# Kernel tuning notes

Measured on AMD Instinct MI355X. Metric: run time of the kernel, lower is better.

## Reference

```python
import jax, jax.numpy as jnp
import numpy as np

N_NODES = 50000
N_EDGES = 800000
IN_DIM = 256
HID_DIM = 128
N_LAYERS = 3


def setup_inputs() -> dict:
    key = jax.random.key(0)
    ks = jax.random.split(key, 7)
    s = 0.05
    x = jax.random.normal(ks[0], (N_NODES, IN_DIM), dtype=jnp.float32)
    edge_index = jax.random.randint(ks[1], (2, N_EDGES), 0, N_NODES, dtype=jnp.int64)
    W_enc = jax.random.normal(ks[2], (HID_DIM, IN_DIM), dtype=jnp.float32) * s
    b_enc = jax.random.normal(ks[3], (HID_DIM,), dtype=jnp.float32) * s
    W_l = jax.random.normal(ks[4], (N_LAYERS, HID_DIM, HID_DIM), dtype=jnp.float32) * s
    b_l = jax.random.normal(ks[5], (N_LAYERS, HID_DIM), dtype=jnp.float32) * s
    W_r = jax.random.normal(ks[6], (N_LAYERS, HID_DIM, HID_DIM), dtype=jnp.float32) * s
    return {"x": x, "edge_index": edge_index, "W_enc": W_enc, "b_enc": b_enc,
            "W_l": W_l, "b_l": b_l, "W_r": W_r}


def reference(x, edge_index, W_enc, b_enc, W_l, b_l, W_r):
    # eval mode: dropout is identity
    n = x.shape[0]
    src, dst = edge_index[0], edge_index[1]
    # encode: Linear(in_dim -> hid_dim)
    h = x @ W_enc.T + b_enc  # [N, H]
    # in-degree for mean aggregation (nodes with no in-edges -> 0 output)
    deg = jax.ops.segment_sum(jnp.ones((src.shape[0],), h.dtype), dst, num_segments=n)
    denom = jnp.maximum(deg, 1.0)[:, None]  # [N, 1]
    for i in range(W_l.shape[0]):
        # mean of source-node features over incoming edges
        agg = jax.ops.segment_sum(h[src], dst, num_segments=n) / denom  # [N, H]
        # SAGEConv: lin_l(agg) + lin_r(h)  (lin_r has no bias)
        h = agg @ W_l[i].T + b_l[i] + h @ W_r[i].T
    return h
```

## Files before the change

kernel.cpp:

```cpp
#include <hip/hip_runtime.h>

#define N_NODES 50000
#define N_EDGES 800000
#define IN_DIM 256
#define HID_DIM 128
#define ROWTILES 3125
#define ENC_BLOCKS 1024
#define WCVT_BLOCKS 48
#define CNT_BLOCKS 256
#define EDGES_PER_CB 3125
#define LYR_GRID 256
#define CAP_E 352
#define TPAD 3136

typedef float f4 __attribute__((ext_vector_type(4)));
typedef float f32x4 __attribute__((ext_vector_type(4)));
typedef float vf2 __attribute__((ext_vector_type(2)));
typedef short bf16x8 __attribute__((ext_vector_type(8)));

__device__ __forceinline__ unsigned short f2bf(float f) {
    unsigned u = __builtin_bit_cast(unsigned, f);
    return (unsigned short)((u + 0x7fffu + ((u >> 16) & 1u)) >> 16);
}
__device__ __forceinline__ unsigned pk2(float a, float b) {
    return (unsigned)f2bf(a) | ((unsigned)f2bf(b) << 16);
}
__device__ __forceinline__ bf16x8 cvt8(f4 a, f4 b) {
    union { bf16x8 v; unsigned u[4]; } r;
    r.u[0] = pk2(a[0], a[1]);
    r.u[1] = pk2(a[2], a[3]);
    r.u[2] = pk2(b[0], b[1]);
    r.u[3] = pk2(b[2], b[3]);
    return r.v;
}
__device__ __forceinline__ vf2 dec8(unsigned short t) {
    return __builtin_amdgcn_cvt_pk_f32_fp8((int)(unsigned)t, false);
}
__device__ __forceinline__ void gl_lds16(const void* g, void* l) {
    __builtin_amdgcn_global_load_lds(
        (const __attribute__((address_space(1))) unsigned int*)g,
        (__attribute__((address_space(3))) unsigned int*)l, 16, 0, 0);
}


__global__ __launch_bounds__(256) void k_pre(const int* __restrict__ dst,
                                             int* __restrict__ Cm,
                                             const float* __restrict__ Wl, const float* __restrict__ Wr,
                                             unsigned short* __restrict__ wlrbf,
                                             const float* __restrict__ x,
                                             const float* __restrict__ Wenc,
                                             const float* __restrict__ bias,
                                             unsigned short* __restrict__ hout,
                                             unsigned char* __restrict__ f8out) {
    __shared__ int smem_i[8192];
    int tid = threadIdx.x;
    if (blockIdx.x < WCVT_BLOCKS) {
        int idx = blockIdx.x * 2048 + tid * 8;
        const float* srcp = (idx < 49152) ? (Wl + idx) : (Wr + (idx - 49152));
        const f4* g = (const f4*)srcp;
        *(bf16x8*)(wlrbf + idx) = cvt8(g[0], g[1]);
        return;
    }
    if (blockIdx.x >= WCVT_BLOCKS + ENC_BLOCKS) {
        int c = blockIdx.x - WCVT_BLOCKS - ENC_BLOCKS;
        int* cnt = smem_i;
        for (int i = tid; i < TPAD; i += 256) cnt[i] = 0;
        __syncthreads();
        const int* dp = dst + c * EDGES_PER_CB;
        for (int i = tid; i < EDGES_PER_CB; i += 256)
            atomicAdd(&cnt[dp[i] >> 4], 1);
        __syncthreads();
        int* crow = Cm + (size_t)c * TPAD;
        for (int t = tid; t < TPAD; t += 256) crow[t] = cnt[t];
        return;
    }
    float* xsf = (float*)smem_i;
    int bid = blockIdx.x - WCVT_BLOCKS;
    int lane = tid & 63;
    int wv = tid >> 6;
    int colbase = wv * 32;
    int lr = lane & 15;
    int kh = (lane >> 4) * 8;
    int khB = kh * 4;
    int swz = (lr & 7) << 4;

    bf16x8 bfr[2][8];
#pragma unroll
    for (int n = 0; n < 2; ++n) {
        const float* wp = Wenc + (size_t)(colbase + n * 16 + lr) * IN_DIM + kh;
#pragma unroll
        for (int s = 0; s < 8; ++s) {
            const f4* g = (const f4*)(wp + s * 32);
            bfr[n][s] = cvt8(g[0], g[1]);
        }
    }
    float bias0 = bias[colbase + lr];
    float bias1 = bias[colbase + 16 + lr];

    int pb = 0;
    for (int rt = bid; rt < ROWTILES; rt += ENC_BLOCKS, pb ^= 1) {
#pragma unroll
        for (int jj = 0; jj < 4; ++jj) {
            int j = wv * 4 + jj;
            const char* gsrc = (const char*)(x + (size_t)(rt * 16 + j) * IN_DIM)
                               + ((lane * 16) ^ ((j & 7) << 4));
            gl_lds16(gsrc, (char*)(xsf + pb * 4096) + j * 1024);
        }
        __syncthreads();

        const char* xb = (const char*)(xsf + pb * 4096) + lr * 1024;
        bf16x8 afr[8];
#pragma unroll
        for (int s = 0; s < 8; ++s) {
            int lo = khB + s * 128;
            f4 a = *(const f4*)(xb + ((lo) ^ swz));
            f4 b = *(const f4*)(xb + ((lo + 16) ^ swz));
            afr[s] = cvt8(a, b);
        }
        f32x4 acc0 = {0.f, 0.f, 0.f, 0.f}, acc1 = {0.f, 0.f, 0.f, 0.f};
#pragma unroll
        for (int s = 0; s < 8; ++s) {
            acc0 = __builtin_amdgcn_mfma_f32_16x16x32_bf16(afr[s], bfr[0][s], acc0, 0, 0, 0);
            acc1 = __builtin_amdgcn_mfma_f32_16x16x32_bf16(afr[s], bfr[1][s], acc1, 0, 0, 0);
        }
        int rbase = rt * 16 + (lane >> 4) * 4;
#pragma unroll
        for (int r = 0; r < 4; ++r) {
            float v0 = acc0[r] + bias0, v1 = acc1[r] + bias1;
            unsigned short* op = hout + (size_t)(rbase + r) * HID_DIM;
            op[colbase + lr] = f2bf(v0);
            op[colbase + 16 + lr] = f2bf(v1);
            unsigned pk = (unsigned)__builtin_amdgcn_cvt_pk_fp8_f32(v0, v1, 0, false);
            unsigned char* fp = f8out + (size_t)(rbase + r) * HID_DIM;
            fp[colbase + lr] = (unsigned char)(pk & 0xff);
            fp[colbase + 16 + lr] = (unsigned char)((pk >> 8) & 0xff);
        }
    }
}


__global__ __launch_bounds__(256) void k_prefix(const int* __restrict__ Cm,
                                                int* __restrict__ STm,
                                                int* __restrict__ tcnt16) {
    int tid = threadIdx.x;
    int lane = tid & 63;
    int t = blockIdx.x * 4 + (tid >> 6);
    if (t >= ROWTILES) return;
    int b0 = lane * 4;
    int c0 = Cm[(size_t)(b0 + 0) * TPAD + t];
    int c1 = Cm[(size_t)(b0 + 1) * TPAD + t];
    int c2 = Cm[(size_t)(b0 + 2) * TPAD + t];
    int c3 = Cm[(size_t)(b0 + 3) * TPAD + t];
    int ls = c0 + c1 + c2 + c3;
    int incl = ls;
#pragma unroll
    for (int off = 1; off < 64; off <<= 1) {
        int v = __shfl_up(incl, off);
        if (lane >= off) incl += v;
    }
    int excl = incl - ls;
    STm[(size_t)(b0 + 0) * TPAD + t] = excl;
    STm[(size_t)(b0 + 1) * TPAD + t] = excl + c0;
    STm[(size_t)(b0 + 2) * TPAD + t] = excl + c0 + c1;
    STm[(size_t)(b0 + 3) * TPAD + t] = excl + c0 + c1 + c2;
    if (lane == 63) tcnt16[t * 16] = incl;
}


__global__ __launch_bounds__(256) void k_scat(const int* __restrict__ src, const int* __restrict__ dst,
                                              const int* __restrict__ STm,
                                              unsigned* __restrict__ buf) {
    __shared__ int sbase[TPAD];
    __shared__ int lcnt[TPAD];
    int tid = threadIdx.x;
    int c = blockIdx.x;
    const int* strow = STm + (size_t)c * TPAD;
    for (int i = tid; i < TPAD; i += 256) { sbase[i] = strow[i]; lcnt[i] = 0; }
    __syncthreads();
    const int* sp = src + c * EDGES_PER_CB;
    const int* dp = dst + c * EDGES_PER_CB;
    for (int i = tid; i < EDGES_PER_CB; i += 256) {
        int sv = sp[i], dv = dp[i];
        int t = dv >> 4, dl = dv & 15;
        int r = atomicAdd(&lcnt[t], 1);
        int slot = sbase[t] + r;
        if (slot < CAP_E) buf[(size_t)t * CAP_E + slot] = (unsigned)sv | ((unsigned)dl << 16);
    }
}


__global__ __launch_bounds__(256) void k_sort2(const unsigned* __restrict__ buf,
                                               const int* __restrict__ tcnt16,
                                               unsigned short* __restrict__ idg,
                                               unsigned short* __restrict__ preft) {
    __shared__ unsigned short stmp[4][512];
    __shared__ int hcur[4][32];
    int tid = threadIdx.x, lane = tid & 63, w = tid >> 6;
    int t = blockIdx.x * 4 + w;
    bool act = t < ROWTILES;
    int cnt = 0;
    if (act) { cnt = tcnt16[t * 16]; if (cnt > CAP_E) cnt = CAP_E; }
    if (lane < 32) hcur[w][lane] = 0;
    unsigned ev[6];
#pragma unroll
    for (int k = 0; k < 6; ++k) {
        int i = lane + k * 64;
        ev[k] = (act && i < cnt) ? buf[(size_t)t * CAP_E + i] : 0xFFFFFFFFu;
    }
    __syncthreads();
#pragma unroll
    for (int k = 0; k < 6; ++k)
        if (ev[k] != 0xFFFFFFFFu) atomicAdd(&hcur[w][ev[k] >> 16], 1);
    __syncthreads();
    int hv = (lane < 16) ? hcur[w][lane] : 0;
    int incl = hv;
#pragma unroll
    for (int off = 1; off <= 16; off <<= 1) {
        int v = __shfl_up(incl, off);
        if (lane >= off) incl += v;
    }
    int excl = incl - hv;
    if (act && lane < 16) hcur[w][16 + lane] = excl;
    if (act && lane <= 16) preft[(size_t)t * 32 + lane] = (unsigned short)excl;
    __syncthreads();
#pragma unroll
    for (int k = 0; k < 6; ++k)
        if (ev[k] != 0xFFFFFFFFu) {
            int r = atomicAdd(&hcur[w][16 + (ev[k] >> 16)], 1);
            stmp[w][r] = (unsigned short)(ev[k] & 0xffff);
        }
    __syncthreads();
    if (act) {
        unsigned* op = (unsigned*)(idg + (size_t)t * 512);
        const unsigned* ip = (const unsigned*)stmp[w];
        int nu = (cnt + 1) >> 1;
        for (int i = lane; i < nu; i += 64) op[i] = ip[i];
    }
}


template <bool LAST>
__global__ __launch_bounds__(256, 1) void k_layer(const unsigned short* __restrict__ H,
                                                  const unsigned char* __restrict__ F8,
                                                  const unsigned short* __restrict__ idg,
                                                  const unsigned short* __restrict__ preft,
                                                  const unsigned short* __restrict__ wlbf,
                                                  const unsigned short* __restrict__ wrbf,
                                                  const float* __restrict__ bias,
                                                  unsigned short* __restrict__ hout,
                                                  unsigned char* __restrict__ f8out,
                                                  float* __restrict__ fout) {
    __shared__ unsigned char rowbuf[2][CAP_E * 128];
    __shared__ unsigned short aggs[16][136];
    __shared__ __align__(16) unsigned short idsb[3][512];
    int tid = threadIdx.x;
    int lane = tid & 63;
    int wv = tid >> 6;
    int colbase = wv * 32;
    int lr = lane & 15;
    int kh = (lane >> 4) * 8;
    int lidx = (lane < 16) ? lane : 16;

    bf16x8 bl[2][4], br[2][4];
#pragma unroll
    for (int n = 0; n < 2; ++n) {
        const unsigned short* lp = wlbf + (size_t)(colbase + n * 16 + lr) * HID_DIM + kh;
        const unsigned short* rp = wrbf + (size_t)(colbase + n * 16 + lr) * HID_DIM + kh;
#pragma unroll
        for (int s = 0; s < 4; ++s) {
            bl[n][s] = *(const bf16x8*)(lp + s * 32);
            br[n][s] = *(const bf16x8*)(rp + s * 32);
        }
    }
    float bias0 = bias[colbase + lr];
    float bias1 = bias[colbase + 16 + lr];

#define ISSUE_GATHER(bsel, ip_, pv) do {                                          \
        int cg_ = __shfl(pv, 16);                                                 \
        int r0_ = __shfl(pv, wv * 4) >> 3;                                        \
        int r1_ = (__shfl(pv, wv * 4 + 4) + 7) >> 3;                              \
        for (int i_ = r0_; i_ < r1_; ++i_) {                                      \
            int ee_ = i_ * 8 + (lane >> 3);                                       \
            ee_ = (ee_ > cg_ - 1) ? cg_ - 1 : ee_;                                \
            const unsigned char* gp_ = F8 + (size_t)idsb[ip_][ee_] * HID_DIM + (lane & 7) * 16; \
            gl_lds16(gp_, &rowbuf[bsel][i_ * 1024]);                              \
        }                                                                         \
    } while (0)

    int rt0 = blockIdx.x;
    gl_lds16((const char*)(idg + (size_t)rt0 * 512) + lane * 16, (void*)idsb[0]);
    if (rt0 + LYR_GRID < ROWTILES)
        gl_lds16((const char*)(idg + (size_t)(rt0 + LYR_GRID) * 512) + lane * 16, (void*)idsb[1]);
    int pc = (int)preft[(size_t)rt0 * 32 + lidx];
    int pn = (rt0 + LYR_GRID < ROWTILES) ? (int)preft[(size_t)(rt0 + LYR_GRID) * 32 + lidx] : 0;
    asm volatile("s_waitcnt vmcnt(0)" ::: "memory");
    __builtin_amdgcn_sched_barrier(0);
    ISSUE_GATHER(0, 0, pc);

    int cur = 0, m = 0;
    for (int rt = rt0; rt < ROWTILES; rt += LYR_GRID) {
        asm volatile("s_waitcnt vmcnt(0)" ::: "memory");
        __builtin_amdgcn_sched_barrier(0);

        if (rt + LYR_GRID < ROWTILES) ISSUE_GATHER(cur ^ 1, (m + 1) % 3, pn);
        if (rt + 2 * LYR_GRID < ROWTILES)
            gl_lds16((const char*)(idg + (size_t)(rt + 2 * LYR_GRID) * 512) + lane * 16,
                     (void*)idsb[(m + 2) % 3]);
        int pn2 = (rt + 2 * LYR_GRID < ROWTILES)
                      ? (int)preft[(size_t)(rt + 2 * LYR_GRID) * 32 + lidx] : 0;
        const unsigned short* hp = H + (size_t)(rt * 16 + lr) * HID_DIM + kh;
        bf16x8 hfr[4];
#pragma unroll
        for (int s = 0; s < 4; ++s) hfr[s] = *(const bf16x8*)(hp + s * 32);

        const unsigned char* rb = rowbuf[cur];
#pragma unroll
        for (int q = 0; q < 4; ++q) {
            int nq = wv * 4 + q;
            int jb = __shfl(pc, nq), je = __shfl(pc, nq + 1);
            float a0 = 0.f, a1 = 0.f;
            int j = jb;
            for (; j + 8 <= je; j += 8) {
                unsigned short t0 = *(const unsigned short*)&rb[(j + 0) * 128 + lane * 2];
                unsigned short t1 = *(const unsigned short*)&rb[(j + 1) * 128 + lane * 2];
                unsigned short t2 = *(const unsigned short*)&rb[(j + 2) * 128 + lane * 2];
                unsigned short t3 = *(const unsigned short*)&rb[(j + 3) * 128 + lane * 2];
                unsigned short t4 = *(const unsigned short*)&rb[(j + 4) * 128 + lane * 2];
                unsigned short t5 = *(const unsigned short*)&rb[(j + 5) * 128 + lane * 2];
                unsigned short t6 = *(const unsigned short*)&rb[(j + 6) * 128 + lane * 2];
                unsigned short t7 = *(const unsigned short*)&rb[(j + 7) * 128 + lane * 2];
                vf2 f0 = dec8(t0), f1 = dec8(t1), f2_ = dec8(t2), f3 = dec8(t3);
                vf2 f4_ = dec8(t4), f5 = dec8(t5), f6 = dec8(t6), f7 = dec8(t7);
                a0 += ((f0[0] + f1[0]) + (f2_[0] + f3[0])) + ((f4_[0] + f5[0]) + (f6[0] + f7[0]));
                a1 += ((f0[1] + f1[1]) + (f2_[1] + f3[1])) + ((f4_[1] + f5[1]) + (f6[1] + f7[1]));
            }
            for (; j + 4 <= je; j += 4) {
                unsigned short t0 = *(const unsigned short*)&rb[(j + 0) * 128 + lane * 2];
                unsigned short t1 = *(const unsigned short*)&rb[(j + 1) * 128 + lane * 2];
                unsigned short t2 = *(const unsigned short*)&rb[(j + 2) * 128 + lane * 2];
                unsigned short t3 = *(const unsigned short*)&rb[(j + 3) * 128 + lane * 2];
                vf2 f0 = dec8(t0), f1 = dec8(t1), f2_ = dec8(t2), f3 = dec8(t3);
                a0 += (f0[0] + f1[0]) + (f2_[0] + f3[0]);
                a1 += (f0[1] + f1[1]) + (f2_[1] + f3[1]);
            }
            for (; j < je; ++j) {
                unsigned short t0 = *(const unsigned short*)&rb[j * 128 + lane * 2];
                vf2 f0 = dec8(t0);
                a0 += f0[0];
                a1 += f0[1];
            }
            int dg = je - jb;
            float inv = 1.0f / (float)(dg > 0 ? dg : 1);
            *(unsigned*)&aggs[nq][lane * 2] = pk2(a0 * inv, a1 * inv);
        }
        __syncthreads();

        bf16x8 afr[4];
#pragma unroll
        for (int s = 0; s < 4; ++s) afr[s] = *(const bf16x8*)&aggs[lr][kh + s * 32];
        f32x4 acc0 = {0.f, 0.f, 0.f, 0.f}, acc1 = {0.f, 0.f, 0.f, 0.f};
#pragma unroll
        for (int s = 0; s < 4; ++s) {
            acc0 = __builtin_amdgcn_mfma_f32_16x16x32_bf16(afr[s], bl[0][s], acc0, 0, 0, 0);
            acc1 = __builtin_amdgcn_mfma_f32_16x16x32_bf16(afr[s], bl[1][s], acc1, 0, 0, 0);
            acc0 = __builtin_amdgcn_mfma_f32_16x16x32_bf16(hfr[s], br[0][s], acc0, 0, 0, 0);
            acc1 = __builtin_amdgcn_mfma_f32_16x16x32_bf16(hfr[s], br[1][s], acc1, 0, 0, 0);
        }
        int rbase = rt * 16 + (lane >> 4) * 4;
#pragma unroll
        for (int r = 0; r < 4; ++r) {
            float v0 = acc0[r] + bias0, v1 = acc1[r] + bias1;
            if (LAST) {
                float* op = fout + (size_t)(rbase + r) * HID_DIM;
                op[colbase + lr] = v0;
                op[colbase + 16 + lr] = v1;
            } else {
                unsigned short* op = hout + (size_t)(rbase + r) * HID_DIM;
                op[colbase + lr] = f2bf(v0);
                op[colbase + 16 + lr] = f2bf(v1);
                unsigned pk = (unsigned)__builtin_amdgcn_cvt_pk_fp8_f32(v0, v1, 0, false);
                unsigned char* fp = f8out + (size_t)(rbase + r) * HID_DIM;
                fp[colbase + lr] = (unsigned char)(pk & 0xff);
                fp[colbase + 16 + lr] = (unsigned char)((pk >> 8) & 0xff);
            }
        }
        __syncthreads();
        pc = pn;
        pn = pn2;
        cur ^= 1;
        m = (m + 1) % 3;
    }
#undef ISSUE_GATHER
}


extern "C" void kernel_launch(void* const* d_in, const int* in_sizes, int n_in,
                              void* d_out, int out_size, void* d_ws, size_t ws_size,
                              hipStream_t stream) {
    const float* x    = (const float*)d_in[0];
    const int*   ei   = (const int*)d_in[1];
    const float* Wenc = (const float*)d_in[2];
    const float* benc = (const float*)d_in[3];
    const float* Wl   = (const float*)d_in[4];
    const float* bl   = (const float*)d_in[5];
    const float* Wr   = (const float*)d_in[6];
    float* out = (float*)d_out;

    const int* srcv = ei;
    const int* dstv = ei + N_EDGES;

    char* p = (char*)d_ws;
    unsigned short* h0    = (unsigned short*)p; p += (size_t)N_NODES * HID_DIM * 2;
    unsigned short* h1    = (unsigned short*)p; p += (size_t)N_NODES * HID_DIM * 2;
    unsigned char*  h0f   = (unsigned char*)p;  p += (size_t)N_NODES * HID_DIM;
    unsigned char*  h1f   = (unsigned char*)p;  p += (size_t)N_NODES * HID_DIM;
    unsigned short* wlrbf = (unsigned short*)p; p += 98304 * 2;
    int*      tcnt16 = (int*)p;      p += 3136 * 16 * 4;
    unsigned short* idg   = (unsigned short*)p; p += (size_t)ROWTILES * 512 * 2;
    unsigned short* preft = (unsigned short*)p; p += (size_t)ROWTILES * 32 * 2;
    unsigned* buf    = (unsigned*)p; p += (size_t)ROWTILES * CAP_E * 4;

    int* Cm  = (int*)h1;
    int* STm = (int*)((char*)h1 + (size_t)CNT_BLOCKS * TPAD * 4);

    unsigned short* wlbf = wlrbf;
    unsigned short* wrbf = wlrbf + 49152;

    k_pre<<<WCVT_BLOCKS + ENC_BLOCKS + CNT_BLOCKS, 256, 0, stream>>>(
        dstv, Cm, Wl, Wr, wlrbf, x, Wenc, benc, h0, h0f);
    k_prefix<<<(ROWTILES + 3) / 4, 256, 0, stream>>>(Cm, STm, tcnt16);
    k_scat<<<CNT_BLOCKS, 256, 0, stream>>>(srcv, dstv, STm, buf);
    k_sort2<<<(ROWTILES + 3) / 4, 256, 0, stream>>>(buf, tcnt16, idg, preft);

    k_layer<false><<<LYR_GRID, 256, 0, stream>>>(h0, h0f, idg, preft, wlbf, wrbf, bl,
                                                 h1, h1f, nullptr);
    k_layer<false><<<LYR_GRID, 256, 0, stream>>>(h1, h1f, idg, preft, wlbf + 16384, wrbf + 16384,
                                                 bl + HID_DIM, h0, h0f, nullptr);
    k_layer<true><<<LYR_GRID, 256, 0, stream>>>(h0, h0f, idg, preft, wlbf + 32768, wrbf + 32768,
                                                bl + 2 * HID_DIM, nullptr, nullptr, out);
}
```

Baseline: 223.4 us.

## Shrink destination tiles to 8 rows to cut LDS and run two blocks per CU

Destination nodes are now bucketed into 8-row tiles instead of 16-row tiles across the counting, prefix, scatter, sort and layer kernels. The per-tile edge buffer capacity drops from 352 to 200, which shrinks the layer kernel's LDS row buffers. That allows launch bounds of two blocks per CU and a grid of 512 blocks, improving latency hiding for the gathers. In exchange, the 16x16 MFMA tiles are half wasted, since lanes 8-15 duplicate rows and only half the lanes store, and the smaller capacity makes overflow truncation more likely on skewed degree distributions.

```diff
diff --git a/kernel.cpp b/kernel.cpp
--- a/kernel.cpp
+++ b/kernel.cpp
@@ -4,14 +4,13 @@
 #define N_EDGES 800000
 #define IN_DIM 256
 #define HID_DIM 128
-#define ROWTILES 3125
+#define ROWTILES8 6250
 #define ENC_BLOCKS 1024
 #define WCVT_BLOCKS 48
 #define CNT_BLOCKS 256
 #define EDGES_PER_CB 3125
-#define LYR_GRID 256
-#define CAP_E 352
-#define TPAD 3136
+#define LYRG 512
+#define CAP8 200
 
 typedef float f4 __attribute__((ext_vector_type(4)));
 typedef float f32x4 __attribute__((ext_vector_type(4)));
@@ -64,14 +63,14 @@
     if (blockIdx.x >= WCVT_BLOCKS + ENC_BLOCKS) {
         int c = blockIdx.x - WCVT_BLOCKS - ENC_BLOCKS;
         int* cnt = smem_i;
-        for (int i = tid; i < TPAD; i += 256) cnt[i] = 0;
+        for (int i = tid; i < ROWTILES8; i += 256) cnt[i] = 0;
         __syncthreads();
         const int* dp = dst + c * EDGES_PER_CB;
         for (int i = tid; i < EDGES_PER_CB; i += 256)
-            atomicAdd(&cnt[dp[i] >> 4], 1);
+            atomicAdd(&cnt[dp[i] >> 3], 1);
         __syncthreads();
-        int* crow = Cm + (size_t)c * TPAD;
-        for (int t = tid; t < TPAD; t += 256) crow[t] = cnt[t];
+        int* crow = Cm + (size_t)c * ROWTILES8;
+        for (int t = tid; t < ROWTILES8; t += 256) crow[t] = cnt[t];
         return;
     }
     float* xsf = (float*)smem_i;
@@ -98,7 +97,7 @@
     float bias1 = bias[colbase + 16 + lr];
 
     int pb = 0;
-    for (int rt = bid; rt < ROWTILES; rt += ENC_BLOCKS, pb ^= 1) {
+    for (int rt = bid; rt < 3125; rt += ENC_BLOCKS, pb ^= 1) {
 #pragma unroll
         for (int jj = 0; jj < 4; ++jj) {
             int j = wv * 4 + jj;
@@ -145,12 +144,12 @@
     int tid = threadIdx.x;
     int lane = tid & 63;
     int t = blockIdx.x * 4 + (tid >> 6);
-    if (t >= ROWTILES) return;
+    if (t >= ROWTILES8) return;
     int b0 = lane * 4;
-    int c0 = Cm[(size_t)(b0 + 0) * TPAD + t];
-    int c1 = Cm[(size_t)(b0 + 1) * TPAD + t];
-    int c2 = Cm[(size_t)(b0 + 2) * TPAD + t];
-    int c3 = Cm[(size_t)(b0 + 3) * TPAD + t];
+    int c0 = Cm[(size_t)(b0 + 0) * ROWTILES8 + t];
+    int c1 = Cm[(size_t)(b0 + 1) * ROWTILES8 + t];
+    int c2 = Cm[(size_t)(b0 + 2) * ROWTILES8 + t];
+    int c3 = Cm[(size_t)(b0 + 3) * ROWTILES8 + t];
     int ls = c0 + c1 + c2 + c3;
     int incl = ls;
 #pragma unroll
@@ -159,10 +158,10 @@
         if (lane >= off) incl += v;
     }
     int excl = incl - ls;
-    STm[(size_t)(b0 + 0) * TPAD + t] = excl;
-    STm[(size_t)(b0 + 1) * TPAD + t] = excl + c0;
-    STm[(size_t)(b0 + 2) * TPAD + t] = excl + c0 + c1;
-    STm[(size_t)(b0 + 3) * TPAD + t] = excl + c0 + c1 + c2;
+    STm[(size_t)(b0 + 0) * ROWTILES8 + t] = excl;
+    STm[(size_t)(b0 + 1) * ROWTILES8 + t] = excl + c0;
+    STm[(size_t)(b0 + 2) * ROWTILES8 + t] = excl + c0 + c1;
+    STm[(size_t)(b0 + 3) * ROWTILES8 + t] = excl + c0 + c1 + c2;
     if (lane == 63) tcnt16[t * 16] = incl;
 }
 
@@ -170,21 +169,21 @@
 __global__ __launch_bounds__(256) void k_scat(const int* __restrict__ src, const int* __restrict__ dst,
                                               const int* __restrict__ STm,
                                               unsigned* __restrict__ buf) {
-    __shared__ int sbase[TPAD];
-    __shared__ int lcnt[TPAD];
+    __shared__ int sbase[ROWTILES8];
+    __shared__ int lcnt[ROWTILES8];
     int tid = threadIdx.x;
     int c = blockIdx.x;
-    const int* strow = STm + (size_t)c * TPAD;
-    for (int i = tid; i < TPAD; i += 256) { sbase[i] = strow[i]; lcnt[i] = 0; }
+    const int* strow = STm + (size_t)c * ROWTILES8;
+    for (int i = tid; i < ROWTILES8; i += 256) { sbase[i] = strow[i]; lcnt[i] = 0; }
     __syncthreads();
     const int* sp = src + c * EDGES_PER_CB;
     const int* dp = dst + c * EDGES_PER_CB;
     for (int i = tid; i < EDGES_PER_CB; i += 256) {
         int sv = sp[i], dv = dp[i];
-        int t = dv >> 4, dl = dv & 15;
+        int t = dv >> 3, dl = dv & 7;
         int r = atomicAdd(&lcnt[t], 1);
         int slot = sbase[t] + r;
-        if (slot < CAP_E) buf[(size_t)t * CAP_E + slot] = (unsigned)sv | ((unsigned)dl << 16);
+        if (slot < CAP8) buf[(size_t)t * CAP8 + slot] = (unsigned)sv | ((unsigned)dl << 16);
     }
 }
 
@@ -193,40 +192,40 @@
                                                const int* __restrict__ tcnt16,
                                                unsigned short* __restrict__ idg,
                                                unsigned short* __restrict__ preft) {
-    __shared__ unsigned short stmp[4][512];
-    __shared__ int hcur[4][32];
+    __shared__ unsigned short stmp[4][256];
+    __shared__ int hc[4][16];
     int tid = threadIdx.x, lane = tid & 63, w = tid >> 6;
     int t = blockIdx.x * 4 + w;
-    bool act = t < ROWTILES;
+    bool act = t < ROWTILES8;
     int cnt = 0;
-    if (act) { cnt = tcnt16[t * 16]; if (cnt > CAP_E) cnt = CAP_E; }
-    if (lane < 32) hcur[w][lane] = 0;
-    unsigned ev[6];
-#pragma unroll
-    for (int k = 0; k < 6; ++k) {
+    if (act) { cnt = tcnt16[t * 16]; if (cnt > CAP8) cnt = CAP8; }
+    if (lane < 16) hc[w][lane] = 0;
+    unsigned ev[4];
+#pragma unroll
+    for (int k = 0; k < 4; ++k) {
         int i = lane + k * 64;
-        ev[k] = (act && i < cnt) ? buf[(size_t)t * CAP_E + i] : 0xFFFFFFFFu;
+        ev[k] = (act && i < cnt) ? buf[(size_t)t * CAP8 + i] : 0xFFFFFFFFu;
     }
     __syncthreads();
 #pragma unroll
-    for (int k = 0; k < 6; ++k)
-        if (ev[k] != 0xFFFFFFFFu) atomicAdd(&hcur[w][ev[k] >> 16], 1);
+    for (int k = 0; k < 4; ++k)
+        if (ev[k] != 0xFFFFFFFFu) atomicAdd(&hc[w][ev[k] >> 16], 1);
     __syncthreads();
-    int hv = (lane < 16) ? hcur[w][lane] : 0;
+    int hv = (lane < 8) ? hc[w][lane] : 0;
     int incl = hv;
 #pragma unroll
-    for (int off = 1; off <= 16; off <<= 1) {
+    for (int off = 1; off <= 8; off <<= 1) {
         int v = __shfl_up(incl, off);
         if (lane >= off) incl += v;
     }
     int excl = incl - hv;
-    if (act && lane < 16) hcur[w][16 + lane] = excl;
-    if (act && lane <= 16) preft[(size_t)t * 32 + lane] = (unsigned short)excl;
+    if (act && lane < 8) hc[w][8 + lane] = excl;
+    if (act && lane <= 8) preft[(size_t)t * 32 + lane] = (unsigned short)excl;
     __syncthreads();
 #pragma unroll
-    for (int k = 0; k < 6; ++k)
+    for (int k = 0; k < 4; ++k)
         if (ev[k] != 0xFFFFFFFFu) {
-            int r = atomicAdd(&hcur[w][16 + (ev[k] >> 16)], 1);
+            int r = atomicAdd(&hc[w][8 + (int)(ev[k] >> 16)], 1);
             stmp[w][r] = (unsigned short)(ev[k] & 0xffff);
         }
     __syncthreads();
@@ -240,7 +239,7 @@
 
 
 template <bool LAST>
-__global__ __launch_bounds__(256, 1) void k_layer(const unsigned short* __restrict__ H,
+__global__ __launch_bounds__(256, 2) void k_layer(const unsigned short* __restrict__ H,
                                                   const unsigned char* __restrict__ F8,
                                                   const unsigned short* __restrict__ idg,
                                                   const unsigned short* __restrict__ preft,
@@ -250,8 +249,8 @@
                                                   unsigned short* __restrict__ hout,
                                                   unsigned char* __restrict__ f8out,
                                                   float* __restrict__ fout) {
-    __shared__ unsigned char rowbuf[2][CAP_E * 128];
-    __shared__ unsigned short aggs[16][136];
+    __shared__ unsigned char rowbuf[2][CAP8 * 128];
+    __shared__ unsigned short aggs[8][136];
     __shared__ __align__(16) unsigned short idsb[3][512];
     int tid = threadIdx.x;
     int lane = tid & 63;
@@ -259,7 +258,7 @@
     int colbase = wv * 32;
     int lr = lane & 15;
     int kh = (lane >> 4) * 8;
-    int lidx = (lane < 16) ? lane : 16;
+    int lidx = (lane < 8) ? lane : 8;
 
     bf16x8 bl[2][4], br[2][4];
 #pragma unroll
@@ -276,9 +275,9 @@
     float bias1 = bias[colbase + 16 + lr];
 
 #define ISSUE_GATHER(bsel, ip_, pv) do {                                          \
-        int cg_ = __shfl(pv, 16);                                                 \
-        int r0_ = __shfl(pv, wv * 4) >> 3;                                        \
-        int r1_ = (__shfl(pv, wv * 4 + 4) + 7) >> 3;                              \
+        int cg_ = __shfl(pv, 8);                                                  \
+        int r0_ = __shfl(pv, wv * 2) >> 3;                                        \
+        int r1_ = (__shfl(pv, wv * 2 + 2) + 7) >> 3;                              \
         for (int i_ = r0_; i_ < r1_; ++i_) {                                      \
             int ee_ = i_ * 8 + (lane >> 3);                                       \
             ee_ = (ee_ > cg_ - 1) ? cg_ - 1 : ee_;                                \
@@ -289,34 +288,34 @@
 
     int rt0 = blockIdx.x;
     gl_lds16((const char*)(idg + (size_t)rt0 * 512) + lane * 16, (void*)idsb[0]);
-    if (rt0 + LYR_GRID < ROWTILES)
-        gl_lds16((const char*)(idg + (size_t)(rt0 + LYR_GRID) * 512) + lane * 16, (void*)idsb[1]);
+    if (rt0 + LYRG < ROWTILES8)
+        gl_lds16((const char*)(idg + (size_t)(rt0 + LYRG) * 512) + lane * 16, (void*)idsb[1]);
     int pc = (int)preft[(size_t)rt0 * 32 + lidx];
-    int pn = (rt0 + LYR_GRID < ROWTILES) ? (int)preft[(size_t)(rt0 + LYR_GRID) * 32 + lidx] : 0;
+    int pn = (rt0 + LYRG < ROWTILES8) ? (int)preft[(size_t)(rt0 + LYRG) * 32 + lidx] : 0;
     asm volatile("s_waitcnt vmcnt(0)" ::: "memory");
     __builtin_amdgcn_sched_barrier(0);
     ISSUE_GATHER(0, 0, pc);
 
     int cur = 0, m = 0;
-    for (int rt = rt0; rt < ROWTILES; rt += LYR_GRID) {
+    for (int rt = rt0; rt < ROWTILES8; rt += LYRG) {
         asm volatile("s_waitcnt vmcnt(0)" ::: "memory");
         __builtin_amdgcn_sched_barrier(0);
 
-        if (rt + LYR_GRID < ROWTILES) ISSUE_GATHER(cur ^ 1, (m + 1) % 3, pn);
-        if (rt + 2 * LYR_GRID < ROWTILES)
-            gl_lds16((const char*)(idg + (size_t)(rt + 2 * LYR_GRID) * 512) + lane * 16,
+        if (rt + LYRG < ROWTILES8) ISSUE_GATHER(cur ^ 1, (m + 1) % 3, pn);
+        if (rt + 2 * LYRG < ROWTILES8)
+            gl_lds16((const char*)(idg + (size_t)(rt + 2 * LYRG) * 512) + lane * 16,
                      (void*)idsb[(m + 2) % 3]);
-        int pn2 = (rt + 2 * LYR_GRID < ROWTILES)
-                      ? (int)preft[(size_t)(rt + 2 * LYR_GRID) * 32 + lidx] : 0;
-        const unsigned short* hp = H + (size_t)(rt * 16 + lr) * HID_DIM + kh;
+        int pn2 = (rt + 2 * LYRG < ROWTILES8)
+                      ? (int)preft[(size_t)(rt + 2 * LYRG) * 32 + lidx] : 0;
+        const unsigned short* hp = H + (size_t)(rt * 8 + (lr & 7)) * HID_DIM + kh;
         bf16x8 hfr[4];
 #pragma unroll
         for (int s = 0; s < 4; ++s) hfr[s] = *(const bf16x8*)(hp + s * 32);
 
         const unsigned char* rb = rowbuf[cur];
 #pragma unroll
-        for (int q = 0; q < 4; ++q) {
-            int nq = wv * 4 + q;
+        for (int q = 0; q < 2; ++q) {
+            int nq = wv * 2 + q;
             int jb = __shfl(pc, nq), je = __shfl(pc, nq + 1);
             float a0 = 0.f, a1 = 0.f;
             int j = jb;
@@ -357,7 +356,7 @@
 
         bf16x8 afr[4];
 #pragma unroll
-        for (int s = 0; s < 4; ++s) afr[s] = *(const bf16x8*)&aggs[lr][kh + s * 32];
+        for (int s = 0; s < 4; ++s) afr[s] = *(const bf16x8*)&aggs[lr & 7][kh + s * 32];
         f32x4 acc0 = {0.f, 0.f, 0.f, 0.f}, acc1 = {0.f, 0.f, 0.f, 0.f};
 #pragma unroll
         for (int s = 0; s < 4; ++s) {
@@ -366,22 +365,24 @@
             acc0 = __builtin_amdgcn_mfma_f32_16x16x32_bf16(hfr[s], br[0][s], acc0, 0, 0, 0);
             acc1 = __builtin_amdgcn_mfma_f32_16x16x32_bf16(hfr[s], br[1][s], acc1, 0, 0, 0);
         }
-        int rbase = rt * 16 + (lane >> 4) * 4;
-#pragma unroll
-        for (int r = 0; r < 4; ++r) {
-            float v0 = acc0[r] + bias0, v1 = acc1[r] + bias1;
-            if (LAST) {
-                float* op = fout + (size_t)(rbase + r) * HID_DIM;
-                op[colbase + lr] = v0;
-                op[colbase + 16 + lr] = v1;
-            } else {
-                unsigned short* op = hout + (size_t)(rbase + r) * HID_DIM;
-                op[colbase + lr] = f2bf(v0);
-                op[colbase + 16 + lr] = f2bf(v1);
-                unsigned pk = (unsigned)__builtin_amdgcn_cvt_pk_fp8_f32(v0, v1, 0, false);
-                unsigned char* fp = f8out + (size_t)(rbase + r) * HID_DIM;
-                fp[colbase + lr] = (unsigned char)(pk & 0xff);
-                fp[colbase + 16 + lr] = (unsigned char)((pk >> 8) & 0xff);
+        if (lane < 32) {
+            int rbase = rt * 8 + (lane >> 4) * 4;
+#pragma unroll
+            for (int r = 0; r < 4; ++r) {
+                float v0 = acc0[r] + bias0, v1 = acc1[r] + bias1;
+                if (LAST) {
+                    float* op = fout + (size_t)(rbase + r) * HID_DIM;
+                    op[colbase + lr] = v0;
+                    op[colbase + 16 + lr] = v1;
+                } else {
+                    unsigned short* op = hout + (size_t)(rbase + r) * HID_DIM;
+                    op[colbase + lr] = f2bf(v0);
+                    op[colbase + 16 + lr] = f2bf(v1);
+                    unsigned pk = (unsigned)__builtin_amdgcn_cvt_pk_fp8_f32(v0, v1, 0, false);
+                    unsigned char* fp = f8out + (size_t)(rbase + r) * HID_DIM;
+                    fp[colbase + lr] = (unsigned char)(pk & 0xff);
+                    fp[colbase + 16 + lr] = (unsigned char)((pk >> 8) & 0xff);
+                }
             }
         }
         __syncthreads();
@@ -415,27 +416,27 @@
     unsigned char*  h0f   = (unsigned char*)p;  p += (size_t)N_NODES * HID_DIM;
     unsigned char*  h1f   = (unsigned char*)p;  p += (size_t)N_NODES * HID_DIM;
     unsigned short* wlrbf = (unsigned short*)p; p += 98304 * 2;
-    int*      tcnt16 = (int*)p;      p += 3136 * 16 * 4;
-    unsigned short* idg   = (unsigned short*)p; p += (size_t)ROWTILES * 512 * 2;
-    unsigned short* preft = (unsigned short*)p; p += (size_t)ROWTILES * 32 * 2;
-    unsigned* buf    = (unsigned*)p; p += (size_t)ROWTILES * CAP_E * 4;
+    int*      tcnt16 = (int*)p;      p += (size_t)6272 * 16 * 4;
+    unsigned short* idg   = (unsigned short*)p; p += (size_t)ROWTILES8 * 512 * 2;
+    unsigned short* preft = (unsigned short*)p; p += (size_t)6272 * 32 * 2;
+    unsigned* buf    = (unsigned*)p; p += (size_t)ROWTILES8 * CAP8 * 4;
 
     int* Cm  = (int*)h1;
-    int* STm = (int*)((char*)h1 + (size_t)CNT_BLOCKS * TPAD * 4);
+    int* STm = (int*)((char*)h1 + (size_t)CNT_BLOCKS * ROWTILES8 * 4);
 
     unsigned short* wlbf = wlrbf;
     unsigned short* wrbf = wlrbf + 49152;
 
     k_pre<<<WCVT_BLOCKS + ENC_BLOCKS + CNT_BLOCKS, 256, 0, stream>>>(
         dstv, Cm, Wl, Wr, wlrbf, x, Wenc, benc, h0, h0f);
-    k_prefix<<<(ROWTILES + 3) / 4, 256, 0, stream>>>(Cm, STm, tcnt16);
+    k_prefix<<<(ROWTILES8 + 3) / 4, 256, 0, stream>>>(Cm, STm, tcnt16);
     k_scat<<<CNT_BLOCKS, 256, 0, stream>>>(srcv, dstv, STm, buf);
-    k_sort2<<<(ROWTILES + 3) / 4, 256, 0, stream>>>(buf, tcnt16, idg, preft);
-
-    k_layer<false><<<LYR_GRID, 256, 0, stream>>>(h0, h0f, idg, preft, wlbf, wrbf, bl,
-                                                 h1, h1f, nullptr);
-    k_layer<false><<<LYR_GRID, 256, 0, stream>>>(h1, h1f, idg, preft, wlbf + 16384, wrbf + 16384,
-                                                 bl + HID_DIM, h0, h0f, nullptr);
-    k_layer<true><<<LYR_GRID, 256, 0, stream>>>(h0, h0f, idg, preft, wlbf + 32768, wrbf + 32768,
-                                                bl + 2 * HID_DIM, nullptr, nullptr, out);
-}
+    k_sort2<<<(ROWTILES8 + 3) / 4, 256, 0, stream>>>(buf, tcnt16, idg, preft);
+
+    k_layer<false><<<LYRG, 256, 0, stream>>>(h0, h0f, idg, preft, wlbf, wrbf, bl,
+                                             h1, h1f, nullptr);
+    k_layer<false><<<LYRG, 256, 0, stream>>>(h1, h1f, idg, preft, wlbf + 16384, wrbf + 16384,
+                                             bl + HID_DIM, h0, h0f, nullptr);
+    k_layer<true><<<LYRG, 256, 0, stream>>>(h0, h0f, idg, preft, wlbf + 32768, wrbf + 32768,
+                                            bl + 2 * HID_DIM, nullptr, nullptr, out);
+}
```

Result: faster. 202.5 us (-9.4%).
